# Optimization experiments

Hardware: AMD Instinct MI355X
Metric: run time of the kernel (lower is better)

The kernel has to match this reference:

```python
import jax, jax.numpy as jnp
import numpy as np
import math

B, S, D, H, R = 4, 2048, 2048, 16, 16
HD = D // H

def setup_inputs() -> dict:
    key = jax.random.key(0)
    ks = jax.random.split(key, 16)
    x = jax.random.normal(ks[0], (B, S, D), dtype=jnp.float32)
    # causal mask: 1 where attendable, 0 where masked (mask==0 -> -1e9)
    mask = jnp.tril(jnp.ones((S, S), dtype=jnp.int32))[None, None, :, :]
    def lin(k):
        return jax.random.normal(k, (D, D), dtype=jnp.float32) / math.sqrt(D)
    def lora(ka, kb):
        A = jax.random.normal(ka, (R, D), dtype=jnp.float32) / math.sqrt(D)
        Bm = jnp.zeros((D, R), dtype=jnp.float32)  # standard LoRA init: B = 0
        return A, Bm
    Aq, Bq = lora(ks[1], ks[2]); Ak, Bk = lora(ks[3], ks[4])
    Av, Bv = lora(ks[5], ks[6]); Ao, Bo = lora(ks[7], ks[8])
    return {"x": x, "mask": mask,
            "Wq": lin(ks[9]), "Aq": Aq, "Bq": Bq,
            "Wk": lin(ks[10]), "Ak": Ak, "Bk": Bk,
            "Wv": lin(ks[11]), "Av": Av, "Bv": Bv,
            "Wo": lin(ks[12]), "Ao": Ao, "Bo": Bo}

def _lora_linear(x, W, A, Bm):
    # y = x @ W^T + (x @ A^T) @ B^T   (LoRA-augmented linear, no bias)
    return x @ W.T + (x @ A.T) @ Bm.T

def reference(x, mask, Wq, Aq, Bq, Wk, Ak, Bk, Wv, Av, Bv, Wo, Ao, Bo):
    b, s, d = x.shape
    def heads(t):
        return t.reshape(b, s, H, HD).transpose(0, 2, 1, 3)  # [B,H,S,HD]
    Q = heads(_lora_linear(x, Wq, Aq, Bq))
    K = heads(_lora_linear(x, Wk, Ak, Bk))
    V = heads(_lora_linear(x, Wv, Av, Bv))
    attn = jnp.einsum('bhqd,bhkd->bhqk', Q, K) / math.sqrt(HD)
    attn = jnp.where(mask == 0, jnp.float32(-1e9), attn)
    attn = jax.nn.softmax(attn, axis=-1)
    out = jnp.einsum('bhqk,bhkd->bhqd', attn, V)  # [B,H,S,HD]
    out = out.transpose(0, 2, 1, 3).reshape(b, s, d)
    return _lora_linear(out, Wo, Ao, Bo)
```

## Files before the change

### kernel.cpp

```cpp
#include <hip/hip_runtime.h>
#include <hip/hip_bf16.h>
#include <stdint.h>


#define L2E 1.4426950408889634f
#define SMSCALE 0.08838834764831845f
#define NEGBIG -3.0e38f

typedef __attribute__((ext_vector_type(4))) float f32x4;
typedef __attribute__((ext_vector_type(16))) float f32x16;
typedef __attribute__((ext_vector_type(8))) __bf16 bfrag;

#if __has_builtin(__builtin_amdgcn_exp2f)
#define EXP2 __builtin_amdgcn_exp2f
#else
#define EXP2 exp2f
#endif

#define DRAIN_VM                                      \
  do {                                                \
    asm volatile("s_waitcnt vmcnt(0)" ::: "memory");  \
    __builtin_amdgcn_sched_barrier(0);                \
  } while (0)

static __device__ __forceinline__ unsigned short f2bf(float f) {
  union { float f; unsigned u; } v; v.f = f;
  unsigned r = v.u + 0x7FFFu + ((v.u >> 16) & 1u);
  return (unsigned short)(r >> 16);
}

static __device__ __forceinline__ void gload16(const void* g, void* l) {
  __builtin_amdgcn_global_load_lds(
      (const __attribute__((address_space(1))) void*)g,
      (__attribute__((address_space(3))) void*)l, 16, 0, 0);
}

__global__ __launch_bounds__(256) void k_fold(const float* __restrict__ W,
                                              const float* __restrict__ A,
                                              const float* __restrict__ Bm,
                                              unsigned short* __restrict__ out) {
  const int n = blockIdx.x;
  const int k0 = threadIdx.x * 8;
  const float* wr = W + (size_t)n * 2048 + k0;
  float acc[8];
#pragma unroll
  for (int j = 0; j < 8; ++j) acc[j] = wr[j];
#pragma unroll 4
  for (int r = 0; r < 16; ++r) {
    float b = Bm[n * 16 + r];
    const float* ar = A + (size_t)r * 2048 + k0;
#pragma unroll
    for (int j = 0; j < 8; ++j) acc[j] = fmaf(b, ar[j], acc[j]);
  }
  unsigned short o[8];
#pragma unroll
  for (int j = 0; j < 8; ++j) o[j] = f2bf(acc[j]);
  *(uint4*)(out + (size_t)n * 2048 + k0) = *(const uint4*)o;
}

__global__ __launch_bounds__(256) void k_cvt(const float* __restrict__ in,
                                             unsigned short* __restrict__ out) {
  const size_t i = ((size_t)blockIdx.x * 256 + threadIdx.x) * 8;
  unsigned short o[8];
#pragma unroll
  for (int j = 0; j < 8; ++j) o[j] = f2bf(in[i + j]);
  *(uint4*)(out + i) = *(const uint4*)o;
}

template <int MODE>
__global__ __launch_bounds__(512, 2) void k_gemm2(const unsigned short* __restrict__ A,
                                                  const unsigned short* __restrict__ Bw,
                                                  void* __restrict__ Cout, float scale) {
  __shared__ __align__(16) unsigned char lds[131072];
  unsigned char* Al = lds;
  unsigned char* Bl = lds + 65536;
  const int tid = threadIdx.x, ln = tid & 63;
  const int w = tid >> 6, g = ln >> 4, cc = ln & 15;
  const int wm = w >> 2, wn = w & 3;
  const int bid = blockIdx.x;
  const int wg = (bid & 7) * 32 + (bid >> 3);
  const int m0 = (wg >> 3) * 256, n0 = (wg & 7) * 256;

  int soff[2], sdst[2];
#pragma unroll
  for (int i = 0; i < 2; ++i) {
    int cid = i * 512 + tid, r = cid >> 2, p = cid & 3;
    int sc = p ^ ((r >> 1) & 3);
    soff[i] = r * 2048 + sc * 8;
    sdst[i] = cid * 16;
  }
  int aro[8], bro[4];
#pragma unroll
  for (int fm = 0; fm < 8; ++fm) {
    int r = wm * 128 + fm * 16 + cc;
    aro[fm] = r * 64 + ((g ^ ((r >> 1) & 3)) << 4);
  }
#pragma unroll
  for (int fn = 0; fn < 4; ++fn) {
    int r = wn * 64 + fn * 16 + cc;
    bro[fn] = r * 64 + ((g ^ ((r >> 1) & 3)) << 4);
  }

#define STAGE_A(b, kt, h)                                                   \
  do {                                                                      \
    _Pragma("unroll")                                                       \
    for (int i = 0; i < 2; ++i)                                             \
      gload16(A + (size_t)m0 * 2048 + soff[i] + (kt) + (h) * 32,            \
              Al + (b) * 32768 + (h) * 16384 + sdst[i]);                    \
  } while (0)
#define STAGE_B(b, kt, h)                                                   \
  do {                                                                      \
    _Pragma("unroll")                                                       \
    for (int i = 0; i < 2; ++i)                                             \
      gload16(Bw + (size_t)n0 * 2048 + soff[i] + (kt) + (h) * 32,           \
              Bl + (b) * 32768 + (h) * 16384 + sdst[i]);                    \
  } while (0)

  f32x4 acc[8][4] = {};

  STAGE_A(0, 0, 0); STAGE_B(0, 0, 0); STAGE_A(0, 0, 1); STAGE_B(0, 0, 1);
  asm volatile("s_waitcnt vmcnt(4)" ::: "memory");
  __builtin_amdgcn_s_barrier();
  __builtin_amdgcn_sched_barrier(0);

  for (int T = 0; T < 32; ++T) {
    const int buf = T & 1;
    const unsigned char* Ab = Al + buf * 32768;
    const unsigned char* Bb = Bl + buf * 32768;
    const int ktn = (T + 1) * 64;
    const bool pf = (T + 1 < 32);
#pragma unroll
    for (int ks = 0; ks < 2; ++ks) {
      bfrag af[8], bf[4];
#pragma unroll
      for (int fm = 0; fm < 8; ++fm)
        af[fm] = *(const bfrag*)(Ab + ks * 16384 + aro[fm]);
#pragma unroll
      for (int j = 0; j < 2; ++j)
        bf[j] = *(const bfrag*)(Bb + ks * 16384 + bro[j]);
      if (pf) STAGE_A(buf ^ 1, ktn, ks);
      __builtin_amdgcn_sched_barrier(0);
      __builtin_amdgcn_s_barrier();
      __builtin_amdgcn_sched_barrier(0);
      __builtin_amdgcn_s_setprio(1);
#pragma unroll
      for (int fm = 0; fm < 8; ++fm)
#pragma unroll
        for (int j = 0; j < 2; ++j)
          acc[fm][j] = __builtin_amdgcn_mfma_f32_16x16x32_bf16(af[fm], bf[j],
                                                               acc[fm][j], 0, 0, 0);
      __builtin_amdgcn_s_setprio(0);
      __builtin_amdgcn_sched_barrier(0);
#pragma unroll
      for (int j = 0; j < 2; ++j)
        bf[2 + j] = *(const bfrag*)(Bb + ks * 16384 + bro[2 + j]);
      if (pf) STAGE_B(buf ^ 1, ktn, ks);
      __builtin_amdgcn_sched_barrier(0);
      asm volatile("s_waitcnt vmcnt(4)" ::: "memory");
      __builtin_amdgcn_s_barrier();
      __builtin_amdgcn_sched_barrier(0);
      __builtin_amdgcn_s_setprio(1);
#pragma unroll
      for (int fm = 0; fm < 8; ++fm)
#pragma unroll
        for (int j = 0; j < 2; ++j)
          acc[fm][2 + j] = __builtin_amdgcn_mfma_f32_16x16x32_bf16(af[fm], bf[2 + j],
                                                                   acc[fm][2 + j], 0, 0, 0);
      __builtin_amdgcn_s_setprio(0);
      __builtin_amdgcn_sched_barrier(0);
    }
  }
#undef STAGE_A
#undef STAGE_B

#pragma unroll
  for (int fm = 0; fm < 8; ++fm)
#pragma unroll
    for (int fn = 0; fn < 4; ++fn)
#pragma unroll
      for (int r = 0; r < 4; ++r) {
        int row = m0 + wm * 128 + fm * 16 + g * 4 + r;
        int col = n0 + wn * 64 + fn * 16 + cc;
        float v = acc[fm][fn][r];
        if (MODE == 0) {
          int b = row >> 11, s = row & 2047, h = col >> 7, hd = col & 127;
          ((unsigned short*)Cout)[(((size_t)b * 16 + h) * 2048 + s) * 128 + hd] =
              f2bf(v * scale);
        } else if (MODE == 2) {
          int b = row >> 11, s = row & 2047, h = col >> 7, hd = col & 127;
          ((unsigned short*)Cout)[(((size_t)b * 16 + h) * 128 + hd) * 2048 + s] =
              f2bf(v);
        } else {
          ((float*)Cout)[(size_t)row * 2048 + col] = v;
        }
      }
}

__global__ __launch_bounds__(512) void k_attn(const unsigned short* __restrict__ Q,
                                              const unsigned short* __restrict__ K,
                                              const unsigned short* __restrict__ Vt,
                                              unsigned short* __restrict__ O) {
  __shared__ __align__(16) unsigned char lds[65536];
  const int tid = threadIdx.x;
  const int ln = tid & 63, w = tid >> 6;
  const int l31 = ln & 31, hi = ln >> 5;
  const int rk = l31 & 15;
  const int bx = blockIdx.x;
  const int gqb = bx >> 6;
  const int qb = (bx < 256) ? (7 - gqb) : (gqb - 4);
  const int bh = bx & 63;
  const int q0 = qb * 256;
  const size_t base = (size_t)bh * 2048 * 128;
  const unsigned short* Qb = Q + base;
  const unsigned short* Kb = K + base;
  const unsigned short* Vb = Vt + base;

  const int qw0 = q0 + w * 32;
  const int qg = qw0 + l31;

  bfrag qf[8];
#pragma unroll
  for (int dc = 0; dc < 8; ++dc)
    qf[dc] = *(const bfrag*)(Qb + (size_t)qg * 128 + dc * 16 + hi * 8);

  f32x16 o[4] = {};
  float m_r = NEGBIG, l_r = 0.f;

  const int nt = q0 / 64 + 4;

  auto stage = [&](int buf, int k0) {
    unsigned char* Kt = lds + buf * 32768;
    unsigned char* Vl = Kt + 16384;
#pragma unroll
    for (int i = 0; i < 2; ++i) {
      int cid = i * 512 + tid;
      int row = cid >> 4, p = cid & 15, sc = p ^ (row & 15);
      gload16(Kb + (size_t)(k0 + row) * 128 + sc * 8, Kt + cid * 16);
    }
#pragma unroll
    for (int i = 0; i < 2; ++i) {
      int cid = i * 512 + tid;
      int row = cid >> 4, p = cid & 15, sc = p ^ (row & 15);
      int d = (sc >> 3) * 64 + row;
      gload16(Vb + (size_t)d * 2048 + k0 + (sc & 7) * 8, Vl + cid * 16);
    }
  };

  stage(0, 0);
  DRAIN_VM;
  __syncthreads();
  int buf = 0;

  for (int t = 0; t < nt; ++t) {
    const int k0 = t * 64;
    if (t + 1 < nt) stage(buf ^ 1, k0 + 64);

    if (k0 <= qw0 + 31) {
      const unsigned char* Kt = lds + buf * 32768;
      const unsigned char* Vl = Kt + 16384;

      f32x16 s0 = {}, s1 = {};
#pragma unroll
      for (int dc = 0; dc < 8; ++dc) {
        int c = dc * 2 + hi;
        bfrag ka = *(const bfrag*)(Kt + (size_t)l31 * 256 + ((c ^ rk) << 4));
        bfrag kb2 = *(const bfrag*)(Kt + (size_t)(32 + l31) * 256 + ((c ^ rk) << 4));
        s0 = __builtin_amdgcn_mfma_f32_32x32x16_bf16(ka, qf[dc], s0, 0, 0, 0);
        s1 = __builtin_amdgcn_mfma_f32_32x32x16_bf16(kb2, qf[dc], s1, 0, 0, 0);
      }

      if (k0 + 63 > qw0) {
#pragma unroll
        for (int r = 0; r < 16; ++r) {
          int ko = (r & 3) + 8 * (r >> 2) + 4 * hi;
          if (k0 + ko > qg) s0[r] = NEGBIG;
          if (k0 + 32 + ko > qg) s1[r] = NEGBIG;
        }
      }

      float pmax = s0[0];
#pragma unroll
      for (int r = 1; r < 16; ++r) pmax = fmaxf(pmax, s0[r]);
#pragma unroll
      for (int r = 0; r < 16; ++r) pmax = fmaxf(pmax, s1[r]);
      pmax = fmaxf(pmax, __shfl_xor(pmax, 32));

      if (!__all(pmax - m_r <= 12.f)) {
        float mn = fmaxf(m_r, pmax);
        float al = EXP2(m_r - mn);
        l_r *= al;
#pragma unroll
        for (int db = 0; db < 4; ++db)
#pragma unroll
          for (int r = 0; r < 16; ++r) o[db][r] *= al;
        m_r = mn;
      }

      unsigned qd0[8], qd1[8];
      float rs = 0.f;
#pragma unroll
      for (int s = 0; s < 4; ++s) {
        float p0 = EXP2(s0[4 * s + 0] - m_r), p1 = EXP2(s0[4 * s + 1] - m_r);
        float p2 = EXP2(s0[4 * s + 2] - m_r), p3 = EXP2(s0[4 * s + 3] - m_r);
        rs += (p0 + p1) + (p2 + p3);
        qd0[2 * s] = (unsigned)f2bf(p0) | ((unsigned)f2bf(p1) << 16);
        qd0[2 * s + 1] = (unsigned)f2bf(p2) | ((unsigned)f2bf(p3) << 16);
      }
#pragma unroll
      for (int s = 0; s < 4; ++s) {
        float p0 = EXP2(s1[4 * s + 0] - m_r), p1 = EXP2(s1[4 * s + 1] - m_r);
        float p2 = EXP2(s1[4 * s + 2] - m_r), p3 = EXP2(s1[4 * s + 3] - m_r);
        rs += (p0 + p1) + (p2 + p3);
        qd1[2 * s] = (unsigned)f2bf(p0) | ((unsigned)f2bf(p1) << 16);
        qd1[2 * s + 1] = (unsigned)f2bf(p2) | ((unsigned)f2bf(p3) << 16);
      }
      rs += __shfl_xor(rs, 32);
      l_r += rs;

#define PVSTEP(QD, B0, KC)                                                    \
  do {                                                                        \
    unsigned e0 = QD[B0], e1 = QD[B0 + 1], x0 = QD[B0 + 2], x1 = QD[B0 + 3];  \
    unsigned kp0 = hi ? x0 : e0, kp1 = hi ? x1 : e1;                          \
    unsigned sd0 = hi ? e0 : x0, sd1 = hi ? e1 : x1;                          \
    unsigned rc0 = (unsigned)__shfl_xor((int)sd0, 32);                        \
    unsigned rc1 = (unsigned)__shfl_xor((int)sd1, 32);                        \
    unsigned pw[4];                                                           \
    pw[0] = hi ? rc0 : kp0; pw[1] = hi ? rc1 : kp1;                           \
    pw[2] = hi ? kp0 : rc0; pw[3] = hi ? kp1 : rc1;                           \
    bfrag pf = *(bfrag*)pw;                                                   \
    _Pragma("unroll")                                                         \
    for (int db = 0; db < 4; ++db) {                                          \
      int c = (db >> 1) * 8 + KC * 2 + hi;                                    \
      bfrag vf = *(const bfrag*)(Vl + (size_t)((db & 1) * 32 + l31) * 256 +   \
                                 ((c ^ rk) << 4));                            \
      o[db] = __builtin_amdgcn_mfma_f32_32x32x16_bf16(vf, pf, o[db], 0, 0, 0);\
    }                                                                         \
  } while (0)

      PVSTEP(qd0, 0, 0);
      PVSTEP(qd0, 4, 1);
      PVSTEP(qd1, 0, 2);
      PVSTEP(qd1, 4, 3);
#undef PVSTEP
    }
    DRAIN_VM;
    __syncthreads();
    buf ^= 1;
  }

  float invl = 1.0f / l_r;
  const int b_ = bh >> 4, h_ = bh & 15;
#pragma unroll
  for (int ph = 0; ph < 2; ++ph) {
    if ((w >> 2) == ph) {
      unsigned char* ep = lds + (w & 3) * 8704;
#pragma unroll
      for (int db = 0; db < 4; ++db)
#pragma unroll
        for (int s = 0; s < 4; ++s) {
          int d0 = db * 32 + 8 * s + 4 * hi;
          float v0 = o[db][4 * s] * invl, v1 = o[db][4 * s + 1] * invl;
          float v2 = o[db][4 * s + 2] * invl, v3 = o[db][4 * s + 3] * invl;
          uint2 pw;
          pw.x = (unsigned)f2bf(v0) | ((unsigned)f2bf(v1) << 16);
          pw.y = (unsigned)f2bf(v2) | ((unsigned)f2bf(v3) << 16);
          *(uint2*)(ep + l31 * 272 + d0 * 2) = pw;
        }
    }
    __syncthreads();
    if ((w >> 2) == ph) {
      const unsigned char* ep = lds + (w & 3) * 8704;
#pragma unroll
      for (int i = 0; i < 8; ++i) {
        int cid = i * 64 + ln;
        int q = cid >> 4, ch = cid & 15;
        uint4 val = *(const uint4*)(ep + q * 272 + ch * 16);
        *(uint4*)(O + ((size_t)(b_ * 2048 + q0 + w * 32 + q)) * 2048 +
                  h_ * 128 + ch * 8) = val;
      }
    }
    __syncthreads();
  }
}

extern "C" void kernel_launch(void* const* d_in, const int* in_sizes, int n_in,
                              void* d_out, int out_size, void* d_ws, size_t ws_size,
                              hipStream_t stream) {
  (void)in_sizes; (void)n_in; (void)out_size; (void)ws_size;
  const float* x  = (const float*)d_in[0];
  const float* Wq = (const float*)d_in[2];
  const float* Aq = (const float*)d_in[3];
  const float* Bq = (const float*)d_in[4];
  const float* Wk = (const float*)d_in[5];
  const float* Ak = (const float*)d_in[6];
  const float* Bk = (const float*)d_in[7];
  const float* Wv = (const float*)d_in[8];
  const float* Av = (const float*)d_in[9];
  const float* Bv = (const float*)d_in[10];
  const float* Wo = (const float*)d_in[11];
  const float* Ao = (const float*)d_in[12];
  const float* Bo = (const float*)d_in[13];

  char* ws = (char*)d_ws;
  unsigned short* xbf = (unsigned short*)ws;
  unsigned short* Wqe = (unsigned short*)(ws + (size_t)33554432);
  unsigned short* Wke = Wqe + 2048 * 2048;
  unsigned short* Wve = Wke + 2048 * 2048;
  unsigned short* Woe = Wve + 2048 * 2048;
  unsigned short* Qb  = (unsigned short*)(ws + (size_t)33554432 + 4u * 8388608u);
  unsigned short* Kb  = Qb + 16777216;
  unsigned short* Vtb = Kb + 16777216;
  unsigned short* AO  = xbf;

  k_fold<<<2048, 256, 0, stream>>>(Wq, Aq, Bq, Wqe);
  k_fold<<<2048, 256, 0, stream>>>(Wk, Ak, Bk, Wke);
  k_fold<<<2048, 256, 0, stream>>>(Wv, Av, Bv, Wve);
  k_fold<<<2048, 256, 0, stream>>>(Wo, Ao, Bo, Woe);
  k_cvt<<<8192, 256, 0, stream>>>(x, xbf);

  k_gemm2<0><<<256, 512, 0, stream>>>(xbf, Wqe, Qb, SMSCALE * L2E);
  k_gemm2<0><<<256, 512, 0, stream>>>(xbf, Wke, Kb, 1.0f);
  k_gemm2<2><<<256, 512, 0, stream>>>(xbf, Wve, Vtb, 1.0f);

  k_attn<<<512, 512, 0, stream>>>(Qb, Kb, Vtb, AO);

  k_gemm2<1><<<256, 512, 0, stream>>>(AO, Woe, d_out, 1.0f);
}
```

Baseline: 422.3 us.

## Batch LoRA folds into one launch, restructure GEMM barriers, simplify attention block order

Merges the four per-weight LoRA fold launches into one 2D-grid launch that takes a pointer struct. In the GEMM main loop, the B fragments are split into two arrays, explicit lgkmcnt waits and extra barriers are added, and the vmcnt wait moves to the end of each k-step. The end of the last tile gets a full vmcnt drain. The attention kernel's query-block ordering changes from a mirrored split to a plain descending order. The extra barriers may add stall time in the GEMM in exchange for stricter LDS-reuse ordering, and the new attention ordering changes how the causal work is balanced across blocks.

```diff
diff --git a/kernel.cpp b/kernel.cpp
--- a/kernel.cpp
+++ b/kernel.cpp
@@ -35,12 +35,19 @@
       (__attribute__((address_space(3))) void*)l, 16, 0, 0);
 }
 
-__global__ __launch_bounds__(256) void k_fold(const float* __restrict__ W,
-                                              const float* __restrict__ A,
-                                              const float* __restrict__ Bm,
-                                              unsigned short* __restrict__ out) {
+struct F4 {
+  const float* W[4];
+  const float* A[4];
+  const float* Bm[4];
+};
+
+__global__ __launch_bounds__(256) void k_fold4(F4 f, unsigned short* __restrict__ out) {
+  const int y = blockIdx.y;
   const int n = blockIdx.x;
   const int k0 = threadIdx.x * 8;
+  const float* W = f.W[y];
+  const float* Aa = f.A[y];
+  const float* Bm = f.Bm[y];
   const float* wr = W + (size_t)n * 2048 + k0;
   float acc[8];
 #pragma unroll
@@ -48,14 +55,14 @@
 #pragma unroll 4
   for (int r = 0; r < 16; ++r) {
     float b = Bm[n * 16 + r];
-    const float* ar = A + (size_t)r * 2048 + k0;
+    const float* ar = Aa + (size_t)r * 2048 + k0;
 #pragma unroll
     for (int j = 0; j < 8; ++j) acc[j] = fmaf(b, ar[j], acc[j]);
   }
   unsigned short o[8];
 #pragma unroll
   for (int j = 0; j < 8; ++j) o[j] = f2bf(acc[j]);
-  *(uint4*)(out + (size_t)n * 2048 + k0) = *(const uint4*)o;
+  *(uint4*)(out + (((size_t)y * 2048 + n) * 2048) + k0) = *(const uint4*)o;
 }
 
 __global__ __launch_bounds__(256) void k_cvt(const float* __restrict__ in,
@@ -118,7 +125,8 @@
 
   f32x4 acc[8][4] = {};
 
-  STAGE_A(0, 0, 0); STAGE_B(0, 0, 0); STAGE_A(0, 0, 1); STAGE_B(0, 0, 1);
+  STAGE_A(0, 0, 0); STAGE_B(0, 0, 0);
+  STAGE_A(0, 0, 1); STAGE_B(0, 0, 1);
   asm volatile("s_waitcnt vmcnt(4)" ::: "memory");
   __builtin_amdgcn_s_barrier();
   __builtin_amdgcn_sched_barrier(0);
@@ -131,43 +139,53 @@
     const bool pf = (T + 1 < 32);
 #pragma unroll
     for (int ks = 0; ks < 2; ++ks) {
-      bfrag af[8], bf[4];
+      bfrag af[8], bf0[2], bf1[2];
 #pragma unroll
       for (int fm = 0; fm < 8; ++fm)
         af[fm] = *(const bfrag*)(Ab + ks * 16384 + aro[fm]);
 #pragma unroll
       for (int j = 0; j < 2; ++j)
-        bf[j] = *(const bfrag*)(Bb + ks * 16384 + bro[j]);
+        bf0[j] = *(const bfrag*)(Bb + ks * 16384 + bro[j]);
       if (pf) STAGE_A(buf ^ 1, ktn, ks);
       __builtin_amdgcn_sched_barrier(0);
       __builtin_amdgcn_s_barrier();
+      asm volatile("s_waitcnt lgkmcnt(0)" ::: "memory");
       __builtin_amdgcn_sched_barrier(0);
       __builtin_amdgcn_s_setprio(1);
 #pragma unroll
       for (int fm = 0; fm < 8; ++fm)
 #pragma unroll
         for (int j = 0; j < 2; ++j)
-          acc[fm][j] = __builtin_amdgcn_mfma_f32_16x16x32_bf16(af[fm], bf[j],
+          acc[fm][j] = __builtin_amdgcn_mfma_f32_16x16x32_bf16(af[fm], bf0[j],
                                                                acc[fm][j], 0, 0, 0);
       __builtin_amdgcn_s_setprio(0);
       __builtin_amdgcn_sched_barrier(0);
+      __builtin_amdgcn_s_barrier();
 #pragma unroll
       for (int j = 0; j < 2; ++j)
-        bf[2 + j] = *(const bfrag*)(Bb + ks * 16384 + bro[2 + j]);
+        bf1[j] = *(const bfrag*)(Bb + ks * 16384 + bro[2 + j]);
       if (pf) STAGE_B(buf ^ 1, ktn, ks);
       __builtin_amdgcn_sched_barrier(0);
-      asm volatile("s_waitcnt vmcnt(4)" ::: "memory");
       __builtin_amdgcn_s_barrier();
+      asm volatile("s_waitcnt lgkmcnt(0)" ::: "memory");
       __builtin_amdgcn_sched_barrier(0);
       __builtin_amdgcn_s_setprio(1);
 #pragma unroll
       for (int fm = 0; fm < 8; ++fm)
 #pragma unroll
         for (int j = 0; j < 2; ++j)
-          acc[fm][2 + j] = __builtin_amdgcn_mfma_f32_16x16x32_bf16(af[fm], bf[2 + j],
+          acc[fm][2 + j] = __builtin_amdgcn_mfma_f32_16x16x32_bf16(af[fm], bf1[j],
                                                                    acc[fm][2 + j], 0, 0, 0);
       __builtin_amdgcn_s_setprio(0);
       __builtin_amdgcn_sched_barrier(0);
+      if (ks == 0) {
+        if (T < 31) asm volatile("s_waitcnt vmcnt(4)" ::: "memory");
+        else        asm volatile("s_waitcnt vmcnt(0)" ::: "memory");
+      } else {
+        if (T < 31) asm volatile("s_waitcnt vmcnt(4)" ::: "memory");
+      }
+      __builtin_amdgcn_sched_barrier(0);
+      __builtin_amdgcn_s_barrier();
     }
   }
 #undef STAGE_A
@@ -206,8 +224,7 @@
   const int l31 = ln & 31, hi = ln >> 5;
   const int rk = l31 & 15;
   const int bx = blockIdx.x;
-  const int gqb = bx >> 6;
-  const int qb = (bx < 256) ? (7 - gqb) : (gqb - 4);
+  const int qb = 7 - (bx >> 6);
   const int bh = bx & 63;
   const int q0 = qb * 256;
   const size_t base = (size_t)bh * 2048 * 128;
@@ -388,41 +405,29 @@
                               hipStream_t stream) {
   (void)in_sizes; (void)n_in; (void)out_size; (void)ws_size;
   const float* x  = (const float*)d_in[0];
-  const float* Wq = (const float*)d_in[2];
-  const float* Aq = (const float*)d_in[3];
-  const float* Bq = (const float*)d_in[4];
-  const float* Wk = (const float*)d_in[5];
-  const float* Ak = (const float*)d_in[6];
-  const float* Bk = (const float*)d_in[7];
-  const float* Wv = (const float*)d_in[8];
-  const float* Av = (const float*)d_in[9];
-  const float* Bv = (const float*)d_in[10];
-  const float* Wo = (const float*)d_in[11];
-  const float* Ao = (const float*)d_in[12];
-  const float* Bo = (const float*)d_in[13];
 
   char* ws = (char*)d_ws;
-  unsigned short* xbf = (unsigned short*)ws;
-  unsigned short* Wqe = (unsigned short*)(ws + (size_t)33554432);
-  unsigned short* Wke = Wqe + 2048 * 2048;
-  unsigned short* Wve = Wke + 2048 * 2048;
-  unsigned short* Woe = Wve + 2048 * 2048;
-  unsigned short* Qb  = (unsigned short*)(ws + (size_t)33554432 + 4u * 8388608u);
-  unsigned short* Kb  = Qb + 16777216;
-  unsigned short* Vtb = Kb + 16777216;
-  unsigned short* AO  = xbf;
-
-  k_fold<<<2048, 256, 0, stream>>>(Wq, Aq, Bq, Wqe);
-  k_fold<<<2048, 256, 0, stream>>>(Wk, Ak, Bk, Wke);
-  k_fold<<<2048, 256, 0, stream>>>(Wv, Av, Bv, Wve);
-  k_fold<<<2048, 256, 0, stream>>>(Wo, Ao, Bo, Woe);
+  unsigned short* xbf  = (unsigned short*)ws;
+  unsigned short* Wall = (unsigned short*)(ws + (size_t)33554432);
+  unsigned short* Qb   = (unsigned short*)(ws + (size_t)67108864);
+  unsigned short* Kb   = Qb + 16777216;
+  unsigned short* Vtb  = Kb + 16777216;
+  unsigned short* AO   = xbf;
+
+  F4 f;
+  f.W[0] = (const float*)d_in[2];  f.A[0] = (const float*)d_in[3];  f.Bm[0] = (const float*)d_in[4];
+  f.W[1] = (const float*)d_in[5];  f.A[1] = (const float*)d_in[6];  f.Bm[1] = (const float*)d_in[7];
+  f.W[2] = (const float*)d_in[8];  f.A[2] = (const float*)d_in[9];  f.Bm[2] = (const float*)d_in[10];
+  f.W[3] = (const float*)d_in[11]; f.A[3] = (const float*)d_in[12]; f.Bm[3] = (const float*)d_in[13];
+
+  k_fold4<<<dim3(2048, 4), 256, 0, stream>>>(f, Wall);
   k_cvt<<<8192, 256, 0, stream>>>(x, xbf);
 
-  k_gemm2<0><<<256, 512, 0, stream>>>(xbf, Wqe, Qb, SMSCALE * L2E);
-  k_gemm2<0><<<256, 512, 0, stream>>>(xbf, Wke, Kb, 1.0f);
-  k_gemm2<2><<<256, 512, 0, stream>>>(xbf, Wve, Vtb, 1.0f);
+  k_gemm2<0><<<256, 512, 0, stream>>>(xbf, Wall, Qb, SMSCALE * L2E);
+  k_gemm2<0><<<256, 512, 0, stream>>>(xbf, Wall + 4194304, Kb, 1.0f);
+  k_gemm2<2><<<256, 512, 0, stream>>>(xbf, Wall + 8388608, Vtb, 1.0f);
 
   k_attn<<<512, 512, 0, stream>>>(Qb, Kb, Vtb, AO);
 
-  k_gemm2<1><<<256, 512, 0, stream>>>(AO, Woe, d_out, 1.0f);
-}
+  k_gemm2<1><<<256, 512, 0, stream>>>(AO, Wall + 12582912, d_out, 1.0f);
+}
```

Measured after the change: 410.2 us. 1.03x faster.
